# Kernel tuning notes

Measured on AMD Instinct MI355X. Metric: run time of the kernel, lower is better.

## Reference

```python
import jax, jax.numpy as jnp
import numpy as np

B = 16
NS = 1024   # coarse points per cloud
NT = 4096   # fine (skip) points per cloud
CIN = 256
CSK = 64
H = 256
K = 3


def setup_inputs() -> dict:
    key = jax.random.key(0)
    ks = jax.random.split(key, 8)
    x = jax.random.normal(ks[0], (B * NS, CIN), dtype=jnp.float32)
    pos = jax.random.normal(ks[1], (B * NS, 3), dtype=jnp.float32)
    x_skip = jax.random.normal(ks[2], (B * NT, CSK), dtype=jnp.float32)
    pos_skip = jax.random.normal(ks[3], (B * NT, 3), dtype=jnp.float32)
    batch = jnp.repeat(jnp.arange(B, dtype=jnp.int64), NS)
    batch_skip = jnp.repeat(jnp.arange(B, dtype=jnp.int64), NT)
    W1 = jax.random.normal(ks[4], (CIN + CSK, H), dtype=jnp.float32) / np.sqrt(CIN + CSK)
    b1 = jnp.zeros((H,), dtype=jnp.float32)
    W2 = jax.random.normal(ks[5], (H, H), dtype=jnp.float32) / np.sqrt(H)
    b2 = jnp.zeros((H,), dtype=jnp.float32)
    return {"x": x, "pos": pos, "x_skip": x_skip, "pos_skip": pos_skip,
            "W1": W1, "b1": b1, "W2": W2, "b2": b2,
            "batch": batch, "batch_skip": batch_skip}


def _knn_interpolate(x, pos, pos_skip):
    # x: [B*NS, C], pos: [B*NS, 3], pos_skip: [B*NT, 3]; equal-size clouds,
    # batch ids are contiguous so per-cloud kNN == reshape to [B, N, .]
    xb = x.reshape(B, NS, -1)
    pb = pos.reshape(B, NS, 3)
    qb = pos_skip.reshape(B, NT, 3)
    # squared distances [B, NT, NS]
    d2 = jnp.sum((qb[:, :, None, :] - pb[:, None, :, :]) ** 2, axis=-1)
    neg_d2k, idx = jax.lax.top_k(-d2, K)            # [B, NT, K]
    w = 1.0 / jnp.maximum(-neg_d2k, 1e-16)          # inverse squared distance
    feats = jax.vmap(lambda xc, ic: xc[ic])(xb, idx)  # [B, NT, K, C]
    y = jnp.sum(feats * w[..., None], axis=2) / jnp.sum(w, axis=2, keepdims=True)
    return y.reshape(B * NT, -1)


def reference(x, pos, x_skip, pos_skip, W1, b1, W2, b2, batch, batch_skip):
    xi = _knn_interpolate(x, pos, pos_skip)          # [B*NT, CIN]
    h = jnp.concatenate([xi, x_skip], axis=1)        # [B*NT, CIN+CSK]
    h = jax.nn.relu(h @ W1 + b1)
    h = jax.nn.relu(h @ W2 + b2)
    return (h, pos_skip, batch_skip)
```

## Files before the change

### kernel.cpp

```cpp
#include <hip/hip_runtime.h>
#include <hip/hip_bf16.h>

#define BB   16
#define NS   1024
#define NT   4096
#define CIN  256
#define CSK  64
#define HD   256
#define K1   (CIN + CSK)
#define MTOT (BB * NT)

typedef __attribute__((ext_vector_type(4))) float f32x4;
typedef __attribute__((ext_vector_type(8))) __bf16 bf16x8;
typedef __attribute__((ext_vector_type(4))) unsigned short ushort4v;

#define W1F_OFF 0u
#define W2F_OFF 163840u

static __device__ __forceinline__ unsigned short f2bf(float f) {
    union { float f; unsigned int u; } v; v.f = f;
    unsigned int r = (v.u + 0x7FFFu + ((v.u >> 16) & 1u)) >> 16;
    return (unsigned short)r;
}
static __device__ __forceinline__ unsigned short f2bf_hw(float f) {
    union { __bf16 b; unsigned short u; } v; v.b = (__bf16)f;
    return v.u;
}

#define PREP_B1 (K1 * HD / 256)
#define PREP_B2 (HD * HD / 256)
#define PREP_B3 ((MTOT * 3) / 256)
__global__ __launch_bounds__(256) void prep_kernel(
    const float* __restrict__ W1, const float* __restrict__ W2,
    const float* __restrict__ pos_skip,
    unsigned short* __restrict__ W1f, unsigned short* __restrict__ W2f,
    float* __restrict__ out)
{
    const int b = blockIdx.x;
    if (b < PREP_B1 + PREP_B2) {
        const bool is1 = b < PREP_B1;
        const int id = (is1 ? b : b - PREP_B1) * 256 + threadIdx.x;
        const int j    = id & 7;
        const int lane = (id >> 3) & 63;
        const int n    = (id >> 9) & 15;
        const int kblk = id >> 13;
        const int k   = kblk * 32 + (lane >> 4) * 8 + j;
        const int col = n * 16 + (lane & 15);
        if (is1) W1f[id] = f2bf(W1[(size_t)k * HD + col]);
        else     W2f[id] = f2bf(W2[(size_t)k * HD + col]);
    } else {
        const int i = (b - PREP_B1 - PREP_B2) * 256 + threadIdx.x;
        const size_t o1 = (size_t)MTOT * HD;
        out[o1 + i] = pos_skip[i];
        if (i < MTOT) out[o1 + (size_t)MTOT * 3 + i] = (float)(i >> 12);
    }
}

__global__ __launch_bounds__(256, 3) void fp_fused_kernel(
    const float* __restrict__ x, const float* __restrict__ x_skip,
    const float* __restrict__ pos, const float* __restrict__ pos_skip,
    const unsigned short* __restrict__ W1f, const unsigned short* __restrict__ W2f,
    const float* __restrict__ b1, const float* __restrict__ b2,
    float* __restrict__ out)
{
    __shared__ __align__(16) unsigned short ldsA[10 * 4 * 512];
    __shared__ int   sidx[64 * 3];
    __shared__ float swgt[64 * 3];

    const int tid = threadIdx.x;
    const int w = tid >> 6, lane = tid & 63;
    const int l15 = lane & 15, lk = lane >> 4;

    const int bid   = blockIdx.x;
    const int xcd   = bid & 7;
    const int j     = bid >> 3;
    const int cloud = xcd + 8 * (j >> 6);
    const int bm    = cloud * 64 + (j & 63);

    {
        float4* sp = (float4*)ldsA;
        const float* pc = pos + (size_t)cloud * NS * 3;
        for (int i = tid; i < NS; i += 256)
            sp[i] = make_float4(pc[i * 3 + 0], pc[i * 3 + 1], pc[i * 3 + 2], 0.f);
        __syncthreads();

        const int qloc = tid >> 2;
        const int p    = tid & 3;
        const int rg   = bm * 64 + qloc;
        const float qx = pos_skip[rg * 3 + 0];
        const float qy = pos_skip[rg * 3 + 1];
        const float qz = pos_skip[rg * 3 + 2];

        double b0 = 1e300, b1k = 1e300, b2k = 1e300;
        double si = (double)p;
        #pragma unroll 4
        for (int i = 0; i < NS / 4; ++i) {
            const int s = i * 4 + p;
            float4 c = sp[s];
            float dx = qx - c.x, dy = qy - c.y, dz = qz - c.z;
            float d = dx * dx + dy * dy + dz * dz;
            double key = fma((double)__float_as_uint(d), 1024.0, si);
            si += 4.0;
            double nb0 = fmin(b0, key);
            double nb1 = fmax(b0, fmin(b1k, key));
            double nb2 = fmax(b1k, fmin(b2k, key));
            b0 = nb0; b1k = nb1; b2k = nb2;
        }
        #pragma unroll
        for (int m = 1; m <= 2; m <<= 1) {
            double o0 = __shfl_xor(b0, m, 64);
            double o1 = __shfl_xor(b1k, m, 64);
            double o2 = __shfl_xor(b2k, m, 64);
            double nb0, nb1, nb2;
            nb0 = fmin(b0, o0); nb1 = fmax(b0, fmin(b1k, o0)); nb2 = fmax(b1k, fmin(b2k, o0));
            b0 = nb0; b1k = nb1; b2k = nb2;
            nb0 = fmin(b0, o1); nb1 = fmax(b0, fmin(b1k, o1)); nb2 = fmax(b1k, fmin(b2k, o1));
            b0 = nb0; b1k = nb1; b2k = nb2;
            nb0 = fmin(b0, o2); nb1 = fmax(b0, fmin(b1k, o2)); nb2 = fmax(b1k, fmin(b2k, o2));
            b0 = nb0; b1k = nb1; b2k = nb2;
        }
        if (p == 0) {
            unsigned long long k0 = (unsigned long long)b0;
            unsigned long long k1 = (unsigned long long)b1k;
            unsigned long long k2 = (unsigned long long)b2k;
            float d0 = __uint_as_float((unsigned int)(k0 >> 10));
            float d1 = __uint_as_float((unsigned int)(k1 >> 10));
            float d2 = __uint_as_float((unsigned int)(k2 >> 10));
            float w0 = 1.f / fmaxf(d0, 1e-16f);
            float w1 = 1.f / fmaxf(d1, 1e-16f);
            float w2 = 1.f / fmaxf(d2, 1e-16f);
            float inv = 1.f / (w0 + w1 + w2);
            sidx[qloc * 3 + 0] = (int)(k0 & 1023ull);
            sidx[qloc * 3 + 1] = (int)(k1 & 1023ull);
            sidx[qloc * 3 + 2] = (int)(k2 & 1023ull);
            swgt[qloc * 3 + 0] = w0 * inv;
            swgt[qloc * 3 + 1] = w1 * inv;
            swgt[qloc * 3 + 2] = w2 * inv;
        }
        __syncthreads();
    }

    {
        const int cb  = cloud * NS;
        const int kbm = lane >> 3;
        const int lkm = (lane >> 1) & 3;
        const int em  = lane & 1;
        const int kbs = 8 + (lane >> 5);
        const int lks = (lane >> 3) & 3;
        const int jjs = lane & 7;
        #pragma unroll 4
        for (int r16 = 0; r16 < 16; ++r16) {
            const int row = w * 16 + r16;
            const int rg  = bm * 64 + row;
            const int i0 = cb + sidx[row * 3 + 0];
            const int i1 = cb + sidx[row * 3 + 1];
            const int i2 = cb + sidx[row * 3 + 2];
            const float w0 = swgt[row * 3 + 0], w1 = swgt[row * 3 + 1], w2 = swgt[row * 3 + 2];
            f32x4 a = *(const f32x4*)(x + (size_t)i0 * CIN + lane * 4);
            f32x4 b = *(const f32x4*)(x + (size_t)i1 * CIN + lane * 4);
            f32x4 c = *(const f32x4*)(x + (size_t)i2 * CIN + lane * 4);
            float s = x_skip[(size_t)rg * CSK + lane];
            f32x4 r = a * w0 + b * w1 + c * w2;
            int H = ((kbm * 4 + w) * 64 + (r16 + 16 * lkm)) * 8 + 4 * em;
            H ^= (kbm & 7) << 3;
            ushort4v o4 = { f2bf_hw(r[0]), f2bf_hw(r[1]), f2bf_hw(r[2]), f2bf_hw(r[3]) };
            *(ushort4v*)&ldsA[H] = o4;
            int H2 = ((kbs * 4 + w) * 64 + (r16 + 16 * lks)) * 8 + jjs;
            H2 ^= (kbs & 7) << 3;
            ldsA[H2] = f2bf_hw(s);
        }
    }
    __syncthreads();

    const unsigned short* w1p = W1f + (w * 4) * 512 + lane * 8;
    const unsigned short* w2p = W2f + (w * 4) * 512 + lane * 8;

    f32x4 acc[4][4];
    #pragma unroll
    for (int mf = 0; mf < 4; ++mf)
        #pragma unroll
        for (int nf = 0; nf < 4; ++nf)
            acc[mf][nf] = f32x4{0.f, 0.f, 0.f, 0.f};

    {
        bf16x8 bc[4], bn[4];
        #pragma unroll
        for (int nf = 0; nf < 4; ++nf)
            bc[nf] = *(const bf16x8*)(w1p + nf * 512);
        #pragma unroll
        for (int kb = 0; kb < 10; ++kb) {
            if (kb < 9) {
                #pragma unroll
                for (int nf = 0; nf < 4; ++nf)
                    bn[nf] = *(const bf16x8*)(w1p + (size_t)(kb + 1) * 8192 + nf * 512);
            }
            bf16x8 a[4];
            #pragma unroll
            for (int mf = 0; mf < 4; ++mf) {
                int aoff = ((kb * 4 + mf) * 64 + lane) * 8;
                aoff ^= (kb & 7) << 3;
                a[mf] = *(const bf16x8*)&ldsA[aoff];
            }
            #pragma unroll
            for (int mf = 0; mf < 4; ++mf)
                #pragma unroll
                for (int nf = 0; nf < 4; ++nf)
                    acc[mf][nf] = __builtin_amdgcn_mfma_f32_16x16x32_bf16(
                        a[mf], bc[nf], acc[mf][nf], 0, 0, 0);
            #pragma unroll
            for (int nf = 0; nf < 4; ++nf) bc[nf] = bn[nf];
        }
    }
    __syncthreads();

    #pragma unroll
    for (int nf = 0; nf < 4; ++nf) {
        const int col = w * 64 + nf * 16 + l15;
        const float bv = b1[col];
        const int kb2   = 2 * w + (nf >> 1);
        const int lane2 = lk * 4 + 16 * ((nf & 1) * 2 + (l15 >> 3));
        #pragma unroll
        for (int mf = 0; mf < 4; ++mf) {
            #pragma unroll
            for (int r = 0; r < 4; ++r) {
                float v = fmaxf(acc[mf][nf][r] + bv, 0.f);
                ldsA[((kb2 * 4 + mf) * 64 + lane2 + r) * 8 + (l15 & 7)] = f2bf_hw(v);
            }
        }
    }
    __syncthreads();

    f32x4 acc2[4][4];
    #pragma unroll
    for (int mf = 0; mf < 4; ++mf)
        #pragma unroll
        for (int nf = 0; nf < 4; ++nf)
            acc2[mf][nf] = f32x4{0.f, 0.f, 0.f, 0.f};

    {
        bf16x8 bc[4], bn[4];
        #pragma unroll
        for (int nf = 0; nf < 4; ++nf)
            bc[nf] = *(const bf16x8*)(w2p + nf * 512);
        #pragma unroll
        for (int kb = 0; kb < 8; ++kb) {
            if (kb < 7) {
                #pragma unroll
                for (int nf = 0; nf < 4; ++nf)
                    bn[nf] = *(const bf16x8*)(w2p + (size_t)(kb + 1) * 8192 + nf * 512);
            }
            bf16x8 a[4];
            #pragma unroll
            for (int mf = 0; mf < 4; ++mf)
                a[mf] = *(const bf16x8*)&ldsA[((kb * 4 + mf) * 64 + lane) * 8];
            #pragma unroll
            for (int mf = 0; mf < 4; ++mf)
                #pragma unroll
                for (int nf = 0; nf < 4; ++nf)
                    acc2[mf][nf] = __builtin_amdgcn_mfma_f32_16x16x32_bf16(
                        a[mf], bc[nf], acc2[mf][nf], 0, 0, 0);
            #pragma unroll
            for (int nf = 0; nf < 4; ++nf) bc[nf] = bn[nf];
        }
    }

    const int rbase = bm * 64 + lk * 4;
    const int cbase = w * 64 + l15;
    #pragma unroll
    for (int nf = 0; nf < 4; ++nf) {
        const int col = cbase + nf * 16;
        const float bv = b2[col];
        #pragma unroll
        for (int mf = 0; mf < 4; ++mf) {
            #pragma unroll
            for (int r = 0; r < 4; ++r) {
                float v = fmaxf(acc2[mf][nf][r] + bv, 0.f);
                out[(size_t)(rbase + mf * 16 + r) * HD + col] = v;
            }
        }
    }
}

extern "C" void kernel_launch(void* const* d_in, const int* in_sizes, int n_in,
                              void* d_out, int out_size, void* d_ws, size_t ws_size,
                              hipStream_t stream)
{
    const float* x        = (const float*)d_in[0];
    const float* pos      = (const float*)d_in[1];
    const float* x_skip   = (const float*)d_in[2];
    const float* pos_skip = (const float*)d_in[3];
    const float* W1       = (const float*)d_in[4];
    const float* b1       = (const float*)d_in[5];
    const float* W2       = (const float*)d_in[6];
    const float* b2       = (const float*)d_in[7];
    float* out = (float*)d_out;

    char* ws = (char*)d_ws;
    unsigned short* W1f  = (unsigned short*)(ws + W1F_OFF);
    unsigned short* W2f  = (unsigned short*)(ws + W2F_OFF);

    prep_kernel<<<PREP_B1 + PREP_B2 + PREP_B3, 256, 0, stream>>>(
        W1, W2, pos_skip, W1f, W2f, out);
    fp_fused_kernel<<<MTOT / 64, 256, 0, stream>>>(
        x, x_skip, pos, pos_skip, W1f, W2f, b1, b2, out);
}
```

Before: 63.42 us.

## Pass kNN indices and weights via wave shuffles instead of LDS, raise occupancy

Each quad keeps its top-3 neighbour indices and normalized weights in registers, and the gather loop fetches them with intra-wave shuffles rather than through shared-memory arrays. This is valid because each wave's 16 query rows are computed by that same wave. The change removes the sidx/swgt LDS arrays, fully unrolls the gather loop, and raises the launch bound's minimum blocks per multiprocessor from 3 to 4 to increase occupancy. The higher occupancy target and full unroll may force register spilling.

```diff
diff --git a/kernel.cpp b/kernel.cpp
--- a/kernel.cpp
+++ b/kernel.cpp
@@ -56,7 +56,7 @@
     }
 }
 
-__global__ __launch_bounds__(256, 3) void fp_fused_kernel(
+__global__ __launch_bounds__(256, 4) void fp_fused_kernel(
     const float* __restrict__ x, const float* __restrict__ x_skip,
     const float* __restrict__ pos, const float* __restrict__ pos_skip,
     const unsigned short* __restrict__ W1f, const unsigned short* __restrict__ W2f,
@@ -64,8 +64,6 @@
     float* __restrict__ out)
 {
     __shared__ __align__(16) unsigned short ldsA[10 * 4 * 512];
-    __shared__ int   sidx[64 * 3];
-    __shared__ float swgt[64 * 3];
 
     const int tid = threadIdx.x;
     const int w = tid >> 6, lane = tid & 63;
@@ -77,6 +75,8 @@
     const int cloud = xcd + 8 * (j >> 6);
     const int bm    = cloud * 64 + (j & 63);
 
+    int   myi0, myi1, myi2;
+    float myw0, myw1, myw2;
     {
         float4* sp = (float4*)ldsA;
         const float* pc = pos + (size_t)cloud * NS * 3;
@@ -84,9 +84,8 @@
             sp[i] = make_float4(pc[i * 3 + 0], pc[i * 3 + 1], pc[i * 3 + 2], 0.f);
         __syncthreads();
 
-        const int qloc = tid >> 2;
-        const int p    = tid & 3;
-        const int rg   = bm * 64 + qloc;
+        const int p  = tid & 3;
+        const int rg = bm * 64 + (tid >> 2);
         const float qx = pos_skip[rg * 3 + 0];
         const float qy = pos_skip[rg * 3 + 1];
         const float qz = pos_skip[rg * 3 + 2];
@@ -119,24 +118,20 @@
             nb0 = fmin(b0, o2); nb1 = fmax(b0, fmin(b1k, o2)); nb2 = fmax(b1k, fmin(b2k, o2));
             b0 = nb0; b1k = nb1; b2k = nb2;
         }
-        if (p == 0) {
-            unsigned long long k0 = (unsigned long long)b0;
-            unsigned long long k1 = (unsigned long long)b1k;
-            unsigned long long k2 = (unsigned long long)b2k;
-            float d0 = __uint_as_float((unsigned int)(k0 >> 10));
-            float d1 = __uint_as_float((unsigned int)(k1 >> 10));
-            float d2 = __uint_as_float((unsigned int)(k2 >> 10));
-            float w0 = 1.f / fmaxf(d0, 1e-16f);
-            float w1 = 1.f / fmaxf(d1, 1e-16f);
-            float w2 = 1.f / fmaxf(d2, 1e-16f);
-            float inv = 1.f / (w0 + w1 + w2);
-            sidx[qloc * 3 + 0] = (int)(k0 & 1023ull);
-            sidx[qloc * 3 + 1] = (int)(k1 & 1023ull);
-            sidx[qloc * 3 + 2] = (int)(k2 & 1023ull);
-            swgt[qloc * 3 + 0] = w0 * inv;
-            swgt[qloc * 3 + 1] = w1 * inv;
-            swgt[qloc * 3 + 2] = w2 * inv;
-        }
+        unsigned long long k0 = (unsigned long long)b0;
+        unsigned long long k1 = (unsigned long long)b1k;
+        unsigned long long k2 = (unsigned long long)b2k;
+        myi0 = (int)(k0 & 1023ull);
+        myi1 = (int)(k1 & 1023ull);
+        myi2 = (int)(k2 & 1023ull);
+        float d0 = __uint_as_float((unsigned int)(k0 >> 10));
+        float d1 = __uint_as_float((unsigned int)(k1 >> 10));
+        float d2 = __uint_as_float((unsigned int)(k2 >> 10));
+        float w0 = 1.f / fmaxf(d0, 1e-16f);
+        float w1 = 1.f / fmaxf(d1, 1e-16f);
+        float w2 = 1.f / fmaxf(d2, 1e-16f);
+        float inv = 1.f / (w0 + w1 + w2);
+        myw0 = w0 * inv; myw1 = w1 * inv; myw2 = w2 * inv;
         __syncthreads();
     }
 
@@ -148,14 +143,17 @@
         const int kbs = 8 + (lane >> 5);
         const int lks = (lane >> 3) & 3;
         const int jjs = lane & 7;
-        #pragma unroll 4
+        #pragma unroll
         for (int r16 = 0; r16 < 16; ++r16) {
+            const int src = r16 * 4;
+            const int i0 = cb + __shfl(myi0, src, 64);
+            const int i1 = cb + __shfl(myi1, src, 64);
+            const int i2 = cb + __shfl(myi2, src, 64);
+            const float w0 = __shfl(myw0, src, 64);
+            const float w1 = __shfl(myw1, src, 64);
+            const float w2 = __shfl(myw2, src, 64);
             const int row = w * 16 + r16;
             const int rg  = bm * 64 + row;
-            const int i0 = cb + sidx[row * 3 + 0];
-            const int i1 = cb + sidx[row * 3 + 1];
-            const int i2 = cb + sidx[row * 3 + 2];
-            const float w0 = swgt[row * 3 + 0], w1 = swgt[row * 3 + 1], w2 = swgt[row * 3 + 2];
             f32x4 a = *(const f32x4*)(x + (size_t)i0 * CIN + lane * 4);
             f32x4 b = *(const f32x4*)(x + (size_t)i1 * CIN + lane * 4);
             f32x4 c = *(const f32x4*)(x + (size_t)i2 * CIN + lane * 4);
```

Measured after the change: 62.84 us, median of 2. About the same (-0.9%).
